# Kernel optimization log

Hardware: AMD Instinct MI355X
Metric: run time of the kernel (lower is better)

The kernel has to match this reference:

```python
import jax, jax.numpy as jnp
import numpy as np

B, N, DIM = 32, 1024, 512
H, KD, ATTN_RATIO = 8, 64, 4
D = ATTN_RATIO * KD            # value dim per head = 256
DH = D * H                     # 2048
QKV_OUT = DH + 2 * H * KD      # 3072
RES = 32                       # resolution (32, 32), N = 32*32
SCALE = KD ** -0.5


def _make_bias_idxs(res):
    coords = np.stack(np.meshgrid(np.arange(res), np.arange(res), indexing="ij"), -1).reshape(-1, 2)  # [N,2]
    off = np.abs(coords[:, None, :] - coords[None, :, :])  # [N,N,2]
    return jnp.asarray(off[..., 0] * res + off[..., 1], dtype=jnp.int32)  # [N,N] in [0, res*res)


def setup_inputs() -> dict:
    key = jax.random.key(0)
    ks = jax.random.split(key, 6)
    x = jax.random.normal(ks[0], (B, N, DIM), dtype=jnp.float32)
    gamma = jnp.ones((DIM,), jnp.float32)
    beta = jnp.zeros((DIM,), jnp.float32)
    qkv_w = jax.random.normal(ks[1], (DIM, QKV_OUT), jnp.float32) * 0.02
    qkv_b = jnp.zeros((QKV_OUT,), jnp.float32)
    proj_w = jax.random.normal(ks[2], (DH, DIM), jnp.float32) * 0.02
    proj_b = jnp.zeros((DIM,), jnp.float32)
    biases = jax.random.normal(ks[3], (H, RES * RES), jnp.float32) * 0.02
    bias_idxs = _make_bias_idxs(RES)
    return {"x": x, "gamma": gamma, "beta": beta, "qkv_w": qkv_w, "qkv_b": qkv_b,
            "proj_w": proj_w, "proj_b": proj_b, "biases": biases, "bias_idxs": bias_idxs}


def reference(x, gamma, beta, qkv_w, qkv_b, proj_w, proj_b, biases, bias_idxs):
    # LayerNorm
    mu = jnp.mean(x, axis=-1, keepdims=True)
    var = jnp.mean(jnp.square(x - mu), axis=-1, keepdims=True)
    xn = (x - mu) * jax.lax.rsqrt(var + 1e-5) * gamma + beta
    # QKV projection and head split
    qkv = (xn @ qkv_w + qkv_b).reshape(B, N, H, 2 * KD + D)
    q, k, v = jnp.split(qkv, [KD, 2 * KD], axis=-1)  # [B,N,H,KD],[B,N,H,KD],[B,N,H,D]
    # Attention with relative-position bias
    bias = biases[:, bias_idxs]  # [H,N,N]
    attn = jnp.einsum("bqhd,bkhd->bhqk", q, k) * SCALE + bias[None]
    attn = jax.nn.softmax(attn, axis=-1)
    out = jnp.einsum("bhqk,bkhd->bqhd", attn, v).reshape(B, N, DH)
    return out @ proj_w + proj_b
```

## Files before the change

### kernel.cpp

```cpp
#include <hip/hip_runtime.h>
#include <hip/hip_bf16.h>
#include <initializer_list>

typedef _Float16 half8 __attribute__((ext_vector_type(8)));
typedef float floatx4 __attribute__((ext_vector_type(4)));

#define MFMA16(a, b, c) __builtin_amdgcn_mfma_f32_16x16x32_f16((a), (b), (c), 0, 0, 0)

__device__ __forceinline__ void gload16(const void* g, void* l) {
    __builtin_amdgcn_global_load_lds((const __attribute__((address_space(1))) unsigned int*)g,
                                     (__attribute__((address_space(3))) unsigned int*)l,
                                     16, 0, 0);
}

__global__ __launch_bounds__(256) void ln_kernel(const float* __restrict__ x,
                                                 const float* __restrict__ gamma,
                                                 const float* __restrict__ beta,
                                                 _Float16* __restrict__ xn) {
    int row = blockIdx.x;
    int tid = threadIdx.x;
    float2 v = ((const float2*)(x + (size_t)row * 512))[tid];

    __shared__ float red[4];
    __shared__ float mv[2];

    float s = v.x + v.y;
#pragma unroll
    for (int o = 32; o > 0; o >>= 1) s += __shfl_down(s, o);
    if ((tid & 63) == 0) red[tid >> 6] = s;
    __syncthreads();
    if (tid == 0) mv[0] = (red[0] + red[1] + red[2] + red[3]) * (1.f / 512.f);
    __syncthreads();
    float mean = mv[0];

    float dx = v.x - mean, dy = v.y - mean;
    float sq = dx * dx + dy * dy;
#pragma unroll
    for (int o = 32; o > 0; o >>= 1) sq += __shfl_xor(sq, o);
    __syncthreads();
    if ((tid & 63) == 0) red[tid >> 6] = sq;
    __syncthreads();
    if (tid == 0) mv[1] = rsqrtf((red[0] + red[1] + red[2] + red[3]) * (1.f / 512.f) + 1e-5f);
    __syncthreads();
    float rstd = mv[1];

    float g0 = gamma[tid * 2], g1 = gamma[tid * 2 + 1];
    float b0 = beta[tid * 2], b1 = beta[tid * 2 + 1];
    union { _Float16 h[2]; unsigned int u; } pk;
    pk.h[0] = (_Float16)(dx * rstd * g0 + b0);
    pk.h[1] = (_Float16)(dy * rstd * g1 + b1);
    ((unsigned int*)(xn + (size_t)row * 512))[tid] = pk.u;
}

__global__ __launch_bounds__(256) void transpose_cast(const float* __restrict__ in,
                                                      _Float16* __restrict__ out,
                                                      int R, int C) {
    __shared__ float t[32][33];
    int c0 = blockIdx.x * 32, r0 = blockIdx.y * 32;
    int tx = threadIdx.x & 31, ty = threadIdx.x >> 5;
#pragma unroll
    for (int j = 0; j < 4; ++j)
        t[ty + j * 8][tx] = in[(size_t)(r0 + ty + j * 8) * C + c0 + tx];
    __syncthreads();
#pragma unroll
    for (int j = 0; j < 4; ++j)
        out[(size_t)(c0 + ty + j * 8) * R + r0 + tx] = (_Float16)t[tx][ty + j * 8];
}

template <int OUTMODE>
__global__ __launch_bounds__(256) void gemm_bt(const _Float16* __restrict__ A,
                                               const _Float16* __restrict__ Bt,
                                               const float* __restrict__ bias,
                                               void* __restrict__ Cout,
                                               _Float16* __restrict__ Vt,
                                               int M, int N, int K) {
    __shared__ __align__(16) _Float16 Asb[128 * 32];
    __shared__ __align__(16) _Float16 Bsb[128 * 32];

    int m0 = blockIdx.x * 128;
    int n0 = blockIdx.y * 128;
    int tid = threadIdx.x;
    int w = tid >> 6, lane = tid & 63, lrow = lane & 15, quad = lane >> 4;
    int wm = (w >> 1) * 64, wn = (w & 1) * 64;

    int srow = lane >> 2;
    int scb = (lane & 3) ^ ((lane >> 3) & 3);
    const _Float16* Abase = A + (size_t)(m0 + w * 16 + srow) * K + scb * 8;
    const _Float16* Bbase = Bt + (size_t)(n0 + w * 16 + srow) * K + scb * 8;
    char* AldsB = (char*)Asb + w * 1024;
    char* BldsB = (char*)Bsb + w * 1024;
    const size_t rowskip = (size_t)64 * K;

    int swz = (lrow >> 1) & 3;

    floatx4 acc[4][4];
#pragma unroll
    for (int i = 0; i < 4; ++i)
#pragma unroll
        for (int j = 0; j < 4; ++j) acc[i][j] = (floatx4){0.f, 0.f, 0.f, 0.f};

    for (int k0 = 0; k0 < K; k0 += 32) {
        __syncthreads();
        gload16(Abase + k0, AldsB);
        gload16(Abase + rowskip + k0, AldsB + 4096);
        gload16(Bbase + k0, BldsB);
        gload16(Bbase + rowskip + k0, BldsB + 4096);
        __syncthreads();

        half8 af[4], bf[4];
#pragma unroll
        for (int i = 0; i < 4; ++i) {
            int r = wm + i * 16 + lrow;
            af[i] = *(const half8*)&Asb[r * 32 + (quad ^ swz) * 8];
        }
#pragma unroll
        for (int j = 0; j < 4; ++j) {
            int r = wn + j * 16 + lrow;
            bf[j] = *(const half8*)&Bsb[r * 32 + (quad ^ swz) * 8];
        }
#pragma unroll
        for (int i = 0; i < 4; ++i)
#pragma unroll
            for (int j = 0; j < 4; ++j)
                acc[i][j] = MFMA16(af[i], bf[j], acc[i][j]);
    }

    int hh = blockIdx.y / 3;
    int part = blockIdx.y - hh * 3;

#pragma unroll
    for (int i = 0; i < 4; ++i)
#pragma unroll
        for (int j = 0; j < 4; ++j) {
            int colg = n0 + wn + j * 16 + lrow;
            int coll = wn + j * 16 + lrow;
            float bv = bias[colg];
#pragma unroll
            for (int r = 0; r < 4; ++r) {
                int rowg = m0 + wm + i * 16 + quad * 4 + r;
                float v = acc[i][j][r] + bv;
                if (OUTMODE == 1) {
                    ((float*)Cout)[(size_t)rowg * N + colg] = v;
                } else {
                    if (part == 0) {
                        ((_Float16*)Cout)[(size_t)rowg * 1024 + hh * 128 + coll] = (_Float16)v;
                    } else {
                        int d = (part - 1) * 128 + coll;
                        int b_rel = rowg >> 10;
                        int n = rowg & 1023;
                        Vt[(((size_t)b_rel * 8 + hh) * 256 + d) * 1024 + n] = (_Float16)v;
                    }
                }
            }
        }
}

__global__ __launch_bounds__(256) void attn_kernel(const _Float16* __restrict__ qk,
                                                   const _Float16* __restrict__ vt,
                                                   const float* __restrict__ biases,
                                                   _Float16* __restrict__ out) {
    int h  = blockIdx.x & 7;
    int qt = (blockIdx.x >> 3) | (blockIdx.y << 1);
    int b  = blockIdx.z;

    int tid = threadIdx.x;
    int w = tid >> 6, lane = tid & 63, lrow = lane & 15, quad = lane >> 4;

    __shared__ float bias_lds[1024];
    __shared__ __align__(16) _Float16 K_lds[32 * 72];
    __shared__ __align__(16) _Float16 V_t[256 * 40];

    const float LOG2E = 1.44269504f;
    for (int i = tid; i < 1024; i += 256) bias_lds[i] = biases[h * 1024 + i] * LOG2E;

    int qrow = qt * 64 + w * 16 + lrow;
    const _Float16* qbase = qk + ((size_t)(b * 1024 + qrow)) * 1024 + h * 128;
    half8 aq0 = *(const half8*)(qbase + quad * 8);
    half8 aq1 = *(const half8*)(qbase + 32 + quad * 8);

    int key_l = tid >> 3, kd8 = (tid & 7) * 8;
    const _Float16* ksrc = qk + ((size_t)(b * 1024 + key_l)) * 1024 + h * 128 + 64 + kd8;
    int cc = tid & 3;
    const _Float16* vsrc0 = vt + ((size_t)((b * 8 + h) * 256 + (tid >> 2))) * 1024 + cc * 4;

    int qr = qrow >> 5, qc = qrow & 31;
    int bcol0[4], bcol1[4];
#pragma unroll
    for (int r = 0; r < 4; ++r) {
        bcol0[r] = abs(qc - (quad * 4 + r));
        bcol1[r] = abs(qc - (16 + quad * 4 + r));
    }

    float m_r = -1e30f, l_r = 0.f;
    floatx4 od[16];
#pragma unroll
    for (int dt = 0; dt < 16; ++dt) od[dt] = (floatx4){0.f, 0.f, 0.f, 0.f};

    uint4 kreg;
    uint2 vA[4], vB[4];

    kreg = *(const uint4*)ksrc;
#pragma unroll
    for (int it = 0; it < 4; ++it) {
        const _Float16* p = vsrc0 + (size_t)it * 64 * 1024;
        vA[it] = *(const uint2*)p;
        vB[it] = *(const uint2*)(p + 16);
    }

    const float SCL = 0.125f * LOG2E;

    for (int kt = 0; kt < 32; ++kt) {
        *(uint4*)&K_lds[key_l * 72 + kd8] = kreg;
#pragma unroll
        for (int it = 0; it < 4; ++it) {
            uint4 v;
            v.x = vA[it].x; v.y = vA[it].y; v.z = vB[it].x; v.w = vB[it].y;
            *(uint4*)&V_t[((tid >> 2) + it * 64) * 40 + cc * 8] = v;
        }
        __syncthreads();

        if (kt < 31) {
            kreg = *(const uint4*)(ksrc + (size_t)(kt + 1) * 32 * 1024);
            const _Float16* vp = vsrc0 + (size_t)(kt + 1) * 32;
#pragma unroll
            for (int it = 0; it < 4; ++it) {
                const _Float16* p = vp + (size_t)it * 64 * 1024;
                vA[it] = *(const uint2*)p;
                vB[it] = *(const uint2*)(p + 16);
            }
        }

        floatx4 sc0 = (floatx4){0.f, 0.f, 0.f, 0.f}, sc1 = sc0;
        {
            half8 kf;
            kf = *(const half8*)&K_lds[lrow * 72 + quad * 8];              sc0 = MFMA16(kf, aq0, sc0);
            kf = *(const half8*)&K_lds[lrow * 72 + 32 + quad * 8];         sc0 = MFMA16(kf, aq1, sc0);
            kf = *(const half8*)&K_lds[(16 + lrow) * 72 + quad * 8];       sc1 = MFMA16(kf, aq0, sc1);
            kf = *(const half8*)&K_lds[(16 + lrow) * 72 + 32 + quad * 8];  sc1 = MFMA16(kf, aq1, sc1);
        }

        int rowoff = abs(qr - kt) << 5;
        float s0[4], s1[4];
#pragma unroll
        for (int r = 0; r < 4; ++r) {
            s0[r] = sc0[r] * SCL + bias_lds[rowoff + bcol0[r]];
            s1[r] = sc1[r] * SCL + bias_lds[rowoff + bcol1[r]];
        }

        float pmax = fmaxf(fmaxf(fmaxf(s0[0], s0[1]), fmaxf(s0[2], s0[3])),
                           fmaxf(fmaxf(s1[0], s1[1]), fmaxf(s1[2], s1[3])));
        pmax = fmaxf(pmax, __shfl_xor(pmax, 16));
        pmax = fmaxf(pmax, __shfl_xor(pmax, 32));

        if (!__all(pmax - m_r <= 8.f)) {
            float mnew = fmaxf(m_r, pmax);
            float alpha = exp2f(m_r - mnew);
            m_r = mnew;
            l_r *= alpha;
            float a4[4];
#pragma unroll
            for (int r = 0; r < 4; ++r) a4[r] = __shfl(alpha, quad * 4 + r, 16);
#pragma unroll
            for (int dt = 0; dt < 16; ++dt)
#pragma unroll
                for (int r = 0; r < 4; ++r) od[dt][r] *= a4[r];
        }

        float p0[4], p1[4], rs = 0.f;
#pragma unroll
        for (int r = 0; r < 4; ++r) { p0[r] = exp2f(s0[r] - m_r); rs += p0[r]; }
#pragma unroll
        for (int r = 0; r < 4; ++r) { p1[r] = exp2f(s1[r] - m_r); rs += p1[r]; }
        rs += __shfl_xor(rs, 16);
        rs += __shfl_xor(rs, 32);
        l_r += rs;

        union { unsigned int u[4]; half8 v; } pa;
        pa.u[0] = __builtin_bit_cast(unsigned int, __builtin_amdgcn_cvt_pkrtz(p0[0], p0[1]));
        pa.u[1] = __builtin_bit_cast(unsigned int, __builtin_amdgcn_cvt_pkrtz(p0[2], p0[3]));
        pa.u[2] = __builtin_bit_cast(unsigned int, __builtin_amdgcn_cvt_pkrtz(p1[0], p1[1]));
        pa.u[3] = __builtin_bit_cast(unsigned int, __builtin_amdgcn_cvt_pkrtz(p1[2], p1[3]));

#pragma unroll
        for (int dt = 0; dt < 16; ++dt) {
            half8 bv = *(const half8*)&V_t[(dt * 16 + lrow) * 40 + quad * 8];
            od[dt] = MFMA16(pa.v, bv, od[dt]);
        }
        __syncthreads();
    }

#pragma unroll
    for (int r = 0; r < 4; ++r) {
        float lq = __shfl(l_r, quad * 4 + r, 16);
        float inv = 1.f / lq;
        int qg = qt * 64 + w * 16 + quad * 4 + r;
        _Float16* orow = out + ((size_t)(b * 1024 + qg)) * 2048 + h * 256;
#pragma unroll
        for (int dt = 0; dt < 16; ++dt)
            orow[dt * 16 + lrow] = (_Float16)(od[dt][r] * inv);
    }
}

extern "C" void kernel_launch(void* const* d_in, const int* in_sizes, int n_in,
                              void* d_out, int out_size, void* d_ws, size_t ws_size,
                              hipStream_t stream) {
    const float* x      = (const float*)d_in[0];
    const float* gamma  = (const float*)d_in[1];
    const float* beta   = (const float*)d_in[2];
    const float* qkv_w  = (const float*)d_in[3];
    const float* qkv_b  = (const float*)d_in[4];
    const float* proj_w = (const float*)d_in[5];
    const float* proj_b = (const float*)d_in[6];
    const float* biases = (const float*)d_in[7];

    float* out = (float*)d_out;

    _Float16* ws      = (_Float16*)d_ws;
    _Float16* qkv_wt  = ws;
    _Float16* proj_wt = qkv_wt + (size_t)512 * 3072;
    _Float16* xn      = proj_wt + (size_t)2048 * 512;
    _Float16* chunk0  = xn + (size_t)32768 * 512;

    const size_t FIXED_HALVES = (size_t)512 * 3072 + (size_t)2048 * 512 + (size_t)32768 * 512;
    int CB = 0;
    for (int cb : {16, 8, 4, 2, 1}) {
        size_t halves = FIXED_HALVES + (size_t)cb * 1024 * (1024 + 2048 + 2048);
        if (halves * sizeof(_Float16) <= ws_size) { CB = cb; break; }
    }
    if (CB == 0) return;
    _Float16* qk_c  = chunk0;
    _Float16* vt_c  = qk_c + (size_t)CB * 1024 * 1024;
    _Float16* att_c = vt_c + (size_t)CB * 1024 * 2048;

    transpose_cast<<<dim3(3072 / 32, 512 / 32), 256, 0, stream>>>(qkv_w, qkv_wt, 512, 3072);
    transpose_cast<<<dim3(512 / 32, 2048 / 32), 256, 0, stream>>>(proj_w, proj_wt, 2048, 512);
    ln_kernel<<<32768, 256, 0, stream>>>(x, gamma, beta, xn);

    const int MC = CB * 1024;
    for (int c = 0; c < 32 / CB; ++c) {
        const _Float16* xn_c = xn + (size_t)c * MC * 512;
        gemm_bt<2><<<dim3(MC / 128, 24), 256, 0, stream>>>(xn_c, qkv_wt, qkv_b,
                                                           (void*)qk_c, vt_c, MC, 3072, 512);
        attn_kernel<<<dim3(16, 8, CB), 256, 0, stream>>>(qk_c, vt_c, biases, att_c);
        float* out_c = out + (size_t)c * MC * 512;
        gemm_bt<1><<<dim3(MC / 128, 4), 256, 0, stream>>>(att_c, proj_wt, proj_b,
                                                          (void*)out_c, nullptr, MC, 512, 2048);
    }
}
```

Baseline: 859.0 us.

## Transpose V-part MFMA in QKV GEMM and simplify attention softmax math

Result: faster. 791.6 us (-7.8%).

```diff
diff --git a/kernel.cpp b/kernel.cpp
--- a/kernel.cpp
+++ b/kernel.cpp
@@ -83,6 +83,14 @@
     int w = tid >> 6, lane = tid & 63, lrow = lane & 15, quad = lane >> 4;
     int wm = (w >> 1) * 64, wn = (w & 1) * 64;
 
+    int hh = 0, part = 0;
+    bool sw = false;
+    if (OUTMODE == 2) {
+        hh = blockIdx.y / 3;
+        part = blockIdx.y - hh * 3;
+        sw = (part != 0);
+    }
+
     int srow = lane >> 2;
     int scb = (lane & 3) ^ ((lane >> 3) & 3);
     const _Float16* Abase = A + (size_t)(m0 + w * 16 + srow) * K + scb * 8;
@@ -118,15 +126,38 @@
             int r = wn + j * 16 + lrow;
             bf[j] = *(const half8*)&Bsb[r * 32 + (quad ^ swz) * 8];
         }
-#pragma unroll
-        for (int i = 0; i < 4; ++i)
-#pragma unroll
-            for (int j = 0; j < 4; ++j)
-                acc[i][j] = MFMA16(af[i], bf[j], acc[i][j]);
-    }
-
-    int hh = blockIdx.y / 3;
-    int part = blockIdx.y - hh * 3;
+        if (OUTMODE == 2 && sw) {
+#pragma unroll
+            for (int i = 0; i < 4; ++i)
+#pragma unroll
+                for (int j = 0; j < 4; ++j)
+                    acc[i][j] = MFMA16(bf[j], af[i], acc[i][j]);
+        } else {
+#pragma unroll
+            for (int i = 0; i < 4; ++i)
+#pragma unroll
+                for (int j = 0; j < 4; ++j)
+                    acc[i][j] = MFMA16(af[i], bf[j], acc[i][j]);
+        }
+    }
+
+    if (OUTMODE == 2 && sw) {
+        int b_rel = m0 >> 10;
+        int tok0 = (m0 & 1023) + wm;
+        _Float16* vbase = Vt + (((size_t)b_rel * 8 + hh) * 256 + (part - 1) * 128) * 1024;
+#pragma unroll
+        for (int j = 0; j < 4; ++j)
+#pragma unroll
+            for (int r = 0; r < 4; ++r) {
+                int d = wn + j * 16 + quad * 4 + r;
+                float bv = bias[n0 + d];
+                _Float16* vrow = vbase + (size_t)d * 1024 + tok0;
+#pragma unroll
+                for (int i = 0; i < 4; ++i)
+                    vrow[i * 16 + lrow] = (_Float16)(acc[i][j][r] + bv);
+            }
+        return;
+    }
 
 #pragma unroll
     for (int i = 0; i < 4; ++i)
@@ -142,14 +173,7 @@
                 if (OUTMODE == 1) {
                     ((float*)Cout)[(size_t)rowg * N + colg] = v;
                 } else {
-                    if (part == 0) {
-                        ((_Float16*)Cout)[(size_t)rowg * 1024 + hh * 128 + coll] = (_Float16)v;
-                    } else {
-                        int d = (part - 1) * 128 + coll;
-                        int b_rel = rowg >> 10;
-                        int n = rowg & 1023;
-                        Vt[(((size_t)b_rel * 8 + hh) * 256 + d) * 1024 + n] = (_Float16)v;
-                    }
+                    ((_Float16*)Cout)[(size_t)rowg * 1024 + hh * 128 + coll] = (_Float16)v;
                 }
             }
         }
@@ -168,10 +192,9 @@
 
     __shared__ float bias_lds[1024];
     __shared__ __align__(16) _Float16 K_lds[32 * 72];
-    __shared__ __align__(16) _Float16 V_t[256 * 40];
-
-    const float LOG2E = 1.44269504f;
-    for (int i = tid; i < 1024; i += 256) bias_lds[i] = biases[h * 1024 + i] * LOG2E;
+    __shared__ __align__(16) _Float16 V_t[256 * 32];
+
+    for (int i = tid; i < 1024; i += 256) bias_lds[i] = biases[h * 1024 + i];
 
     int qrow = qt * 64 + w * 16 + lrow;
     const _Float16* qbase = qk + ((size_t)(b * 1024 + qrow)) * 1024 + h * 128;
@@ -207,15 +230,13 @@
         vB[it] = *(const uint2*)(p + 16);
     }
 
-    const float SCL = 0.125f * LOG2E;
-
     for (int kt = 0; kt < 32; ++kt) {
         *(uint4*)&K_lds[key_l * 72 + kd8] = kreg;
 #pragma unroll
         for (int it = 0; it < 4; ++it) {
             uint4 v;
             v.x = vA[it].x; v.y = vA[it].y; v.z = vB[it].x; v.w = vB[it].y;
-            *(uint4*)&V_t[((tid >> 2) + it * 64) * 40 + cc * 8] = v;
+            *(uint4*)&V_t[((tid >> 2) + it * 64) * 32 + cc * 8] = v;
         }
         __syncthreads();
 
@@ -243,8 +264,8 @@
         float s0[4], s1[4];
 #pragma unroll
         for (int r = 0; r < 4; ++r) {
-            s0[r] = sc0[r] * SCL + bias_lds[rowoff + bcol0[r]];
-            s1[r] = sc1[r] * SCL + bias_lds[rowoff + bcol1[r]];
+            s0[r] = sc0[r] * 0.125f + bias_lds[rowoff + bcol0[r]];
+            s1[r] = sc1[r] * 0.125f + bias_lds[rowoff + bcol1[r]];
         }
 
         float pmax = fmaxf(fmaxf(fmaxf(s0[0], s0[1]), fmaxf(s0[2], s0[3])),
@@ -254,7 +275,7 @@
 
         if (!__all(pmax - m_r <= 8.f)) {
             float mnew = fmaxf(m_r, pmax);
-            float alpha = exp2f(m_r - mnew);
+            float alpha = __expf(m_r - mnew);
             m_r = mnew;
             l_r *= alpha;
             float a4[4];
@@ -268,22 +289,20 @@
 
         float p0[4], p1[4], rs = 0.f;
 #pragma unroll
-        for (int r = 0; r < 4; ++r) { p0[r] = exp2f(s0[r] - m_r); rs += p0[r]; }
-#pragma unroll
-        for (int r = 0; r < 4; ++r) { p1[r] = exp2f(s1[r] - m_r); rs += p1[r]; }
+        for (int r = 0; r < 4; ++r) { p0[r] = __expf(s0[r] - m_r); rs += p0[r]; }
+#pragma unroll
+        for (int r = 0; r < 4; ++r) { p1[r] = __expf(s1[r] - m_r); rs += p1[r]; }
         rs += __shfl_xor(rs, 16);
         rs += __shfl_xor(rs, 32);
         l_r += rs;
 
-        union { unsigned int u[4]; half8 v; } pa;
-        pa.u[0] = __builtin_bit_cast(unsigned int, __builtin_amdgcn_cvt_pkrtz(p0[0], p0[1]));
-        pa.u[1] = __builtin_bit_cast(unsigned int, __builtin_amdgcn_cvt_pkrtz(p0[2], p0[3]));
-        pa.u[2] = __builtin_bit_cast(unsigned int, __builtin_amdgcn_cvt_pkrtz(p1[0], p1[1]));
-        pa.u[3] = __builtin_bit_cast(unsigned int, __builtin_amdgcn_cvt_pkrtz(p1[2], p1[3]));
+        union H8 { _Float16 h[8]; half8 v; } pa;
+#pragma unroll
+        for (int r = 0; r < 4; ++r) { pa.h[r] = (_Float16)p0[r]; pa.h[4 + r] = (_Float16)p1[r]; }
 
 #pragma unroll
         for (int dt = 0; dt < 16; ++dt) {
-            half8 bv = *(const half8*)&V_t[(dt * 16 + lrow) * 40 + quad * 8];
+            half8 bv = *(const half8*)&V_t[(dt * 16 + lrow) * 32 + quad * 8];
             od[dt] = MFMA16(pa.v, bv, od[dt]);
         }
         __syncthreads();
```
